# Optimization experiments

Measured on AMD Instinct MI355X. Metric: run time of the kernel, lower is better.

The kernel has to match this reference:

```python
import jax, jax.numpy as jnp
from jax import lax
import numpy as np

IN, HID, OUT = 28, 64, 10


def _lstm_layer(x_seq, W_ih, W_hh, b_ih, b_hh):
    # x_seq: [B, T, in]; PyTorch gate order: i, f, g, o (stacked along 4H)
    B = x_seq.shape[0]
    H = W_hh.shape[1]
    # Precompute input projection for all timesteps: [B, T, 4H]
    x_proj = jnp.einsum('bti,gi->btg', x_seq, W_ih) + b_ih + b_hh

    def step(carry, xt):
        h, c = carry
        gates = xt + h @ W_hh.T  # [B, 4H]
        i, f, g, o = jnp.split(gates, 4, axis=-1)
        i = jax.nn.sigmoid(i)
        f = jax.nn.sigmoid(f)
        g = jnp.tanh(g)
        o = jax.nn.sigmoid(o)
        c = f * c + i * g
        h = o * jnp.tanh(c)
        return (h, c), h

    h0 = jnp.zeros((B, H), x_seq.dtype)
    (_, _), hs = lax.scan(step, (h0, h0), jnp.swapaxes(x_proj, 0, 1))
    return jnp.swapaxes(hs, 0, 1)  # [B, T, H]


def setup_inputs() -> dict:
    key = jax.random.key(0)
    ks = jax.random.split(key, 12)
    s_in = 1.0 / np.sqrt(HID)
    u = lambda k, shape: jax.random.uniform(k, shape, jnp.float32, -s_in, s_in)
    return {
        'x': jax.random.normal(ks[0], (16384, 1, 28, 28), jnp.float32),
        'W_ih0': u(ks[1], (4 * HID, IN)),
        'W_hh0': u(ks[2], (4 * HID, HID)),
        'b_ih0': u(ks[3], (4 * HID,)),
        'b_hh0': u(ks[4], (4 * HID,)),
        'W_ih1': u(ks[5], (4 * HID, HID)),
        'W_hh1': u(ks[6], (4 * HID, HID)),
        'b_ih1': u(ks[7], (4 * HID,)),
        'b_hh1': u(ks[8], (4 * HID,)),
        'W_lin': u(ks[9], (OUT, HID)),
        'b_lin': u(ks[10], (OUT,)),
    }


def reference(x, W_ih0, W_hh0, b_ih0, b_hh0, W_ih1, W_hh1, b_ih1, b_hh1, W_lin, b_lin):
    # (N, C, H, W) -> (N, C*H, W): sequence of rows, feature = W = 28
    x = x.reshape(x.shape[0], -1, x.shape[-1])
    h1 = _lstm_layer(x, W_ih0, W_hh0, b_ih0, b_hh0)   # [B, T, 64]
    h2 = _lstm_layer(h1, W_ih1, W_hh1, b_ih1, b_hh1)  # [B, T, 64]
    last = h2[:, -1, :]
    return last @ W_lin.T + b_lin  # [B, 10]
```

## Files before the change

kernel.cpp:

```cpp
#include <hip/hip_runtime.h>


typedef _Float16 half8 __attribute__((ext_vector_type(8)));
typedef float floatx4 __attribute__((ext_vector_type(4)));

__device__ __forceinline__ float sigf(float v) {
    return __builtin_amdgcn_rcpf(1.0f + __expf(-v));
}
__device__ __forceinline__ float tanhf2(float v) {
    return 1.0f - 2.0f * __builtin_amdgcn_rcpf(__expf(2.0f * v) + 1.0f);
}

__launch_bounds__(1024, 4)
__global__ void lstm_mfma(const float* __restrict__ x,
                          const float* __restrict__ Wih0, const float* __restrict__ Whh0,
                          const float* __restrict__ bih0, const float* __restrict__ bhh0,
                          const float* __restrict__ Wih1, const float* __restrict__ Whh1,
                          const float* __restrict__ bih1, const float* __restrict__ bhh1,
                          const float* __restrict__ Wlin, const float* __restrict__ blin,
                          float* __restrict__ out) {
    __shared__ __align__(16) _Float16 h0p[2][4096];
    __shared__ __align__(16) _Float16 h1p[2][4096];
    __shared__ __align__(16) _Float16 xb[2][2048];
    __shared__ float wlin_s[640];
    __shared__ float blin_s[10];

    const int lane = threadIdx.x;
    const int w    = threadIdx.y;
    const int tid  = w * 64 + lane;
    const int mtg  = w >> 1;
    const int ntg  = w & 1;
    const int quad = lane >> 4;
    const int col  = lane & 15;

    half8 A0[2][3], A1[2][4];
    #pragma unroll
    for (int im = 0; im < 2; ++im) {
        int mt = mtg * 2 + im;
        int m  = mt * 16 + col;
        int u  = m >> 2, g = m & 3;
        int row = g * 64 + u;
        #pragma unroll
        for (int kt = 0; kt < 3; ++kt) {
            half8 r;
            #pragma unroll
            for (int j = 0; j < 8; ++j) {
                int k = kt * 32 + quad * 8 + j;
                float v;
                if (k < 28)       v = Wih0[row * 28 + k];
                else if (k == 28) v = bih0[row] + bhh0[row];
                else if (k < 32)  v = 0.f;
                else              v = Whh0[row * 64 + (k - 32)];
                r[j] = (_Float16)v;
            }
            A0[im][kt] = r;
        }
        #pragma unroll
        for (int kt = 0; kt < 4; ++kt) {
            half8 r;
            #pragma unroll
            for (int j = 0; j < 8; ++j) {
                int k = kt * 32 + quad * 8 + j;
                float v = (k < 64) ? Wih1[row * 64 + k] : Whh1[row * 64 + (k - 64)];
                r[j] = (_Float16)v;
            }
            A1[im][kt] = r;
        }
    }
    floatx4 bias1[2];
    #pragma unroll
    for (int im = 0; im < 2; ++im) {
        int u = (mtg * 2 + im) * 4 + quad;
        #pragma unroll
        for (int r = 0; r < 4; ++r) bias1[im][r] = bih1[r * 64 + u] + bhh1[r * 64 + u];
    }

    int xrd[2], hrd[2][2], hwr[2][2];
    #pragma unroll
    for (int in = 0; in < 2; ++in) {
        int nt = ntg * 2 + in;
        xrd[in] = nt * 512 + lane * 8;
        #pragma unroll
        for (int kt = 0; kt < 2; ++kt) hrd[kt][in] = (nt * 2 + kt) * 512 + lane * 8;
        #pragma unroll
        for (int im = 0; im < 2; ++im) {
            int u = (mtg * 2 + im) * 4 + quad;
            hwr[im][in] = (nt * 2 + (u >> 5)) * 512 + (((u >> 3) & 3) * 16 + col) * 8 + (u & 7);
        }
    }

    const int xi = tid & 31;
    const bool xvalid = xi < 28;
    const float* xg[2];
    int xstg[2];
    #pragma unroll
    for (int s = 0; s < 2; ++s) {
        int b = (tid >> 5) + s * 32;
        xg[s]   = x + (blockIdx.x * 64 + b) * 784 + xi;
        xstg[s] = (b >> 4) * 512 + ((xi >> 3) * 16 + (b & 15)) * 8 + (xi & 7);
    }

    {
        int* z0 = (int*)&h0p[0][0];
        int* z1 = (int*)&h1p[0][0];
        #pragma unroll
        for (int i = tid; i < 2048; i += 1024) { z0[i] = 0; z1[i] = 0; }
        #pragma unroll
        for (int s = 0; s < 2; ++s) {
            float xv = xvalid ? xg[s][0] : 0.f;
            xb[0][xstg[s]] = (xi == 28) ? (_Float16)1.0f : (_Float16)xv;
        }
    }
    __syncthreads();

    float c0[4] = {0.f, 0.f, 0.f, 0.f};
    float c1[4] = {0.f, 0.f, 0.f, 0.f};

    for (int t = 0; t < 28; ++t) {
        const int p = t & 1, q = p ^ 1;
        _Float16* h0r = h0p[p];
        _Float16* h0w = h0p[q];
        _Float16* h1r = h1p[p];
        _Float16* h1w = h1p[q];
        const _Float16* xr = xb[p];

        float xn[2] = {0.f, 0.f};
        if (t < 27) {
            #pragma unroll
            for (int s = 0; s < 2; ++s)
                if (xvalid) xn[s] = xg[s][(t + 1) * 28];
        }

        floatx4 acc[2][2];
        #pragma unroll
        for (int im = 0; im < 2; ++im)
            #pragma unroll
            for (int in = 0; in < 2; ++in)
                acc[im][in] = (floatx4){0.f, 0.f, 0.f, 0.f};

        #pragma unroll
        for (int in = 0; in < 2; ++in) {
            half8 bf = *(const half8*)&xr[xrd[in]];
            #pragma unroll
            for (int im = 0; im < 2; ++im)
                acc[im][in] = __builtin_amdgcn_mfma_f32_16x16x32_f16(A0[im][0], bf, acc[im][in], 0, 0, 0);
        }
        #pragma unroll
        for (int kt = 0; kt < 2; ++kt) {
            #pragma unroll
            for (int in = 0; in < 2; ++in) {
                half8 bf = *(const half8*)&h0r[hrd[kt][in]];
                #pragma unroll
                for (int im = 0; im < 2; ++im)
                    acc[im][in] = __builtin_amdgcn_mfma_f32_16x16x32_f16(A0[im][kt + 1], bf, acc[im][in], 0, 0, 0);
            }
        }
        #pragma unroll
        for (int im = 0; im < 2; ++im) {
            #pragma unroll
            for (int in = 0; in < 2; ++in) {
                floatx4 a = acc[im][in];
                float ig = sigf(a[0]), fg = sigf(a[1]), gg = tanhf2(a[2]), og = sigf(a[3]);
                float c = fg * c0[im * 2 + in] + ig * gg;
                c0[im * 2 + in] = c;
                h0w[hwr[im][in]] = (_Float16)(og * tanhf2(c));
            }
        }
        __syncthreads();

        #pragma unroll
        for (int im = 0; im < 2; ++im)
            #pragma unroll
            for (int in = 0; in < 2; ++in)
                acc[im][in] = bias1[im];

        #pragma unroll
        for (int kt = 0; kt < 2; ++kt) {
            #pragma unroll
            for (int in = 0; in < 2; ++in) {
                half8 bf = *(const half8*)&h0w[hrd[kt][in]];
                #pragma unroll
                for (int im = 0; im < 2; ++im)
                    acc[im][in] = __builtin_amdgcn_mfma_f32_16x16x32_f16(A1[im][kt], bf, acc[im][in], 0, 0, 0);
            }
        }
        #pragma unroll
        for (int kt = 0; kt < 2; ++kt) {
            #pragma unroll
            for (int in = 0; in < 2; ++in) {
                half8 bf = *(const half8*)&h1r[hrd[kt][in]];
                #pragma unroll
                for (int im = 0; im < 2; ++im)
                    acc[im][in] = __builtin_amdgcn_mfma_f32_16x16x32_f16(A1[im][kt + 2], bf, acc[im][in], 0, 0, 0);
            }
        }
        #pragma unroll
        for (int im = 0; im < 2; ++im) {
            #pragma unroll
            for (int in = 0; in < 2; ++in) {
                floatx4 a = acc[im][in];
                float ig = sigf(a[0]), fg = sigf(a[1]), gg = tanhf2(a[2]), og = sigf(a[3]);
                float c = fg * c1[im * 2 + in] + ig * gg;
                c1[im * 2 + in] = c;
                h1w[hwr[im][in]] = (_Float16)(og * tanhf2(c));
            }
        }
        if (t < 27) {
            #pragma unroll
            for (int s = 0; s < 2; ++s)
                xb[q][xstg[s]] = (xi == 28) ? (_Float16)1.0f : (_Float16)xn[s];
        }
        __syncthreads();
    }

    if (tid < 640) wlin_s[tid] = Wlin[tid];
    if (tid < 10)  blin_s[tid] = blin[tid];
    __syncthreads();
    if (tid < 640) {
        int b = tid / 10, o = tid - b * 10;
        float a = blin_s[o];
        #pragma unroll 8
        for (int u = 0; u < 64; ++u) {
            float hv = (float)h1p[0][((b >> 4) * 2 + (u >> 5)) * 512 + (((u >> 3) & 3) * 16 + (b & 15)) * 8 + (u & 7)];
            a += wlin_s[o * 64 + u] * hv;
        }
        out[(blockIdx.x * 64 + b) * 10 + o] = a;
    }
}

extern "C" void kernel_launch(void* const* d_in, const int* in_sizes, int n_in,
                              void* d_out, int out_size, void* d_ws, size_t ws_size,
                              hipStream_t stream) {
    const float* x    = (const float*)d_in[0];
    const float* Wih0 = (const float*)d_in[1];
    const float* Whh0 = (const float*)d_in[2];
    const float* bih0 = (const float*)d_in[3];
    const float* bhh0 = (const float*)d_in[4];
    const float* Wih1 = (const float*)d_in[5];
    const float* Whh1 = (const float*)d_in[6];
    const float* bih1 = (const float*)d_in[7];
    const float* bhh1 = (const float*)d_in[8];
    const float* Wlin = (const float*)d_in[9];
    const float* blin = (const float*)d_in[10];
    float* out = (float*)d_out;

    lstm_mfma<<<256, dim3(64, 16), 0, stream>>>(x, Wih0, Whh0, bih0, bhh0,
                                                Wih1, Whh1, bih1, bhh1, Wlin, blin, out);
}
```

Baseline: 205.2 us.

## Halve batch per block to 32 and hoist layer-1 recurrent MFMAs before barrier

Each block now handles 32 sequences with 8 waves instead of 64 with 16, which doubles the grid to 512 blocks and halves LDS per block. The intent is to spread work over more CUs, since 256 blocks underfill the device. The layer-1 recurrent product on h1 from the previous step is also moved ahead of the layer-0 activation and barrier, so its MFMAs can overlap with layer-0 work. In exchange each wave holds a second accumulator set, which raises register pressure.

```diff
diff --git a/kernel.cpp b/kernel.cpp
--- a/kernel.cpp
+++ b/kernel.cpp
@@ -11,7 +11,7 @@
     return 1.0f - 2.0f * __builtin_amdgcn_rcpf(__expf(2.0f * v) + 1.0f);
 }
 
-__launch_bounds__(1024, 4)
+__launch_bounds__(512, 4)
 __global__ void lstm_mfma(const float* __restrict__ x,
                           const float* __restrict__ Wih0, const float* __restrict__ Whh0,
                           const float* __restrict__ bih0, const float* __restrict__ bhh0,
@@ -19,24 +19,22 @@
                           const float* __restrict__ bih1, const float* __restrict__ bhh1,
                           const float* __restrict__ Wlin, const float* __restrict__ blin,
                           float* __restrict__ out) {
-    __shared__ __align__(16) _Float16 h0p[2][4096];
-    __shared__ __align__(16) _Float16 h1p[2][4096];
-    __shared__ __align__(16) _Float16 xb[2][2048];
+    __shared__ __align__(16) _Float16 h0p[2][2048];
+    __shared__ __align__(16) _Float16 h1p[2][2048];
+    __shared__ __align__(16) _Float16 xb[2][1024];
     __shared__ float wlin_s[640];
     __shared__ float blin_s[10];
 
     const int lane = threadIdx.x;
     const int w    = threadIdx.y;
     const int tid  = w * 64 + lane;
-    const int mtg  = w >> 1;
-    const int ntg  = w & 1;
     const int quad = lane >> 4;
     const int col  = lane & 15;
 
     half8 A0[2][3], A1[2][4];
     #pragma unroll
     for (int im = 0; im < 2; ++im) {
-        int mt = mtg * 2 + im;
+        int mt = 2 * w + im;
         int m  = mt * 16 + col;
         int u  = m >> 2, g = m & 3;
         int row = g * 64 + u;
@@ -70,7 +68,7 @@
     floatx4 bias1[2];
     #pragma unroll
     for (int im = 0; im < 2; ++im) {
-        int u = (mtg * 2 + im) * 4 + quad;
+        int u = (2 * w + im) * 4 + quad;
         #pragma unroll
         for (int r = 0; r < 4; ++r) bias1[im][r] = bih1[r * 64 + u] + bhh1[r * 64 + u];
     }
@@ -78,14 +76,13 @@
     int xrd[2], hrd[2][2], hwr[2][2];
     #pragma unroll
     for (int in = 0; in < 2; ++in) {
-        int nt = ntg * 2 + in;
-        xrd[in] = nt * 512 + lane * 8;
-        #pragma unroll
-        for (int kt = 0; kt < 2; ++kt) hrd[kt][in] = (nt * 2 + kt) * 512 + lane * 8;
+        xrd[in] = in * 512 + lane * 8;
+        #pragma unroll
+        for (int kt = 0; kt < 2; ++kt) hrd[kt][in] = (in * 2 + kt) * 512 + lane * 8;
         #pragma unroll
         for (int im = 0; im < 2; ++im) {
-            int u = (mtg * 2 + im) * 4 + quad;
-            hwr[im][in] = (nt * 2 + (u >> 5)) * 512 + (((u >> 3) & 3) * 16 + col) * 8 + (u & 7);
+            int u = (2 * w + im) * 4 + quad;
+            hwr[im][in] = (in * 2 + (u >> 5)) * 512 + (((u >> 3) & 3) * 16 + col) * 8 + (u & 7);
         }
     }
 
@@ -95,8 +92,8 @@
     int xstg[2];
     #pragma unroll
     for (int s = 0; s < 2; ++s) {
-        int b = (tid >> 5) + s * 32;
-        xg[s]   = x + (blockIdx.x * 64 + b) * 784 + xi;
+        int b = (tid >> 5) + s * 16;
+        xg[s]   = x + (blockIdx.x * 32 + b) * 784 + xi;
         xstg[s] = (b >> 4) * 512 + ((xi >> 3) * 16 + (b & 15)) * 8 + (xi & 7);
     }
 
@@ -104,7 +101,7 @@
         int* z0 = (int*)&h0p[0][0];
         int* z1 = (int*)&h1p[0][0];
         #pragma unroll
-        for (int i = tid; i < 2048; i += 1024) { z0[i] = 0; z1[i] = 0; }
+        for (int i = tid; i < 1024; i += 512) { z0[i] = 0; z1[i] = 0; }
         #pragma unroll
         for (int s = 0; s < 2; ++s) {
             float xv = xvalid ? xg[s][0] : 0.f;
@@ -131,19 +128,19 @@
                 if (xvalid) xn[s] = xg[s][(t + 1) * 28];
         }
 
-        floatx4 acc[2][2];
+        floatx4 acc0[2][2], acc1[2][2];
         #pragma unroll
         for (int im = 0; im < 2; ++im)
             #pragma unroll
             for (int in = 0; in < 2; ++in)
-                acc[im][in] = (floatx4){0.f, 0.f, 0.f, 0.f};
+                acc0[im][in] = (floatx4){0.f, 0.f, 0.f, 0.f};
 
         #pragma unroll
         for (int in = 0; in < 2; ++in) {
             half8 bf = *(const half8*)&xr[xrd[in]];
             #pragma unroll
             for (int im = 0; im < 2; ++im)
-                acc[im][in] = __builtin_amdgcn_mfma_f32_16x16x32_f16(A0[im][0], bf, acc[im][in], 0, 0, 0);
+                acc0[im][in] = __builtin_amdgcn_mfma_f32_16x16x32_f16(A0[im][0], bf, acc0[im][in], 0, 0, 0);
         }
         #pragma unroll
         for (int kt = 0; kt < 2; ++kt) {
@@ -152,14 +149,31 @@
                 half8 bf = *(const half8*)&h0r[hrd[kt][in]];
                 #pragma unroll
                 for (int im = 0; im < 2; ++im)
-                    acc[im][in] = __builtin_amdgcn_mfma_f32_16x16x32_f16(A0[im][kt + 1], bf, acc[im][in], 0, 0, 0);
-            }
-        }
+                    acc0[im][in] = __builtin_amdgcn_mfma_f32_16x16x32_f16(A0[im][kt + 1], bf, acc0[im][in], 0, 0, 0);
+            }
+        }
+
+        #pragma unroll
+        for (int im = 0; im < 2; ++im)
+            #pragma unroll
+            for (int in = 0; in < 2; ++in)
+                acc1[im][in] = bias1[im];
+        #pragma unroll
+        for (int kt = 0; kt < 2; ++kt) {
+            #pragma unroll
+            for (int in = 0; in < 2; ++in) {
+                half8 bf = *(const half8*)&h1r[hrd[kt][in]];
+                #pragma unroll
+                for (int im = 0; im < 2; ++im)
+                    acc1[im][in] = __builtin_amdgcn_mfma_f32_16x16x32_f16(A1[im][kt + 2], bf, acc1[im][in], 0, 0, 0);
+            }
+        }
+
         #pragma unroll
         for (int im = 0; im < 2; ++im) {
             #pragma unroll
             for (int in = 0; in < 2; ++in) {
-                floatx4 a = acc[im][in];
+                floatx4 a = acc0[im][in];
                 float ig = sigf(a[0]), fg = sigf(a[1]), gg = tanhf2(a[2]), og = sigf(a[3]);
                 float c = fg * c0[im * 2 + in] + ig * gg;
                 c0[im * 2 + in] = c;
@@ -169,36 +183,21 @@
         __syncthreads();
 
         #pragma unroll
-        for (int im = 0; im < 2; ++im)
-            #pragma unroll
-            for (int in = 0; in < 2; ++in)
-                acc[im][in] = bias1[im];
-
-        #pragma unroll
         for (int kt = 0; kt < 2; ++kt) {
             #pragma unroll
             for (int in = 0; in < 2; ++in) {
                 half8 bf = *(const half8*)&h0w[hrd[kt][in]];
                 #pragma unroll
                 for (int im = 0; im < 2; ++im)
-                    acc[im][in] = __builtin_amdgcn_mfma_f32_16x16x32_f16(A1[im][kt], bf, acc[im][in], 0, 0, 0);
-            }
-        }
-        #pragma unroll
-        for (int kt = 0; kt < 2; ++kt) {
-            #pragma unroll
-            for (int in = 0; in < 2; ++in) {
-                half8 bf = *(const half8*)&h1r[hrd[kt][in]];
-                #pragma unroll
-                for (int im = 0; im < 2; ++im)
-                    acc[im][in] = __builtin_amdgcn_mfma_f32_16x16x32_f16(A1[im][kt + 2], bf, acc[im][in], 0, 0, 0);
-            }
-        }
+                    acc1[im][in] = __builtin_amdgcn_mfma_f32_16x16x32_f16(A1[im][kt], bf, acc1[im][in], 0, 0, 0);
+            }
+        }
+
         #pragma unroll
         for (int im = 0; im < 2; ++im) {
             #pragma unroll
             for (int in = 0; in < 2; ++in) {
-                floatx4 a = acc[im][in];
+                floatx4 a = acc1[im][in];
                 float ig = sigf(a[0]), fg = sigf(a[1]), gg = tanhf2(a[2]), og = sigf(a[3]);
                 float c = fg * c1[im * 2 + in] + ig * gg;
                 c1[im * 2 + in] = c;
@@ -213,10 +212,11 @@
         __syncthreads();
     }
 
-    if (tid < 640) wlin_s[tid] = Wlin[tid];
-    if (tid < 10)  blin_s[tid] = blin[tid];
+    #pragma unroll
+    for (int i = tid; i < 640; i += 512) wlin_s[i] = Wlin[i];
+    if (tid < 10) blin_s[tid] = blin[tid];
     __syncthreads();
-    if (tid < 640) {
+    if (tid < 320) {
         int b = tid / 10, o = tid - b * 10;
         float a = blin_s[o];
         #pragma unroll 8
@@ -224,7 +224,7 @@
             float hv = (float)h1p[0][((b >> 4) * 2 + (u >> 5)) * 512 + (((u >> 3) & 3) * 16 + (b & 15)) * 8 + (u & 7)];
             a += wlin_s[o * 64 + u] * hv;
         }
-        out[(blockIdx.x * 64 + b) * 10 + o] = a;
+        out[(blockIdx.x * 32 + b) * 10 + o] = a;
     }
 }
 
@@ -244,6 +244,6 @@
     const float* blin = (const float*)d_in[10];
     float* out = (float*)d_out;
 
-    lstm_mfma<<<256, dim3(64, 16), 0, stream>>>(x, Wih0, Whh0, bih0, bhh0,
-                                                Wih1, Whh1, bih1, bhh1, Wlin, blin, out);
-}
+    lstm_mfma<<<512, dim3(64, 8), 0, stream>>>(x, Wih0, Whh0, bih0, bhh0,
+                                               Wih1, Whh1, bih1, bhh1, Wlin, blin, out);
+}
```

New measurement: 202.0 us. Within noise of the previous version (-1.5%).
